# Kernel optimization log

Hardware: AMD Instinct MI355X
Metric: run time of the kernel (lower is better)

## Reference

```python
import jax, jax.numpy as jnp
import numpy as np

MARGIN = 0.2
W_HARD = 1.0
W_SOFT = 0.0
NORMALIZE = True
PD_EPS = 1e-6  # torch F.pairwise_distance eps used inside TripletMarginLoss


def setup_inputs() -> dict:
    key = jax.random.key(0)
    k1, k2, k3 = jax.random.split(key, 3)
    N, D = 8192, 128
    z = jax.random.normal(k1, (N, D), dtype=jnp.float32)
    labels = jax.random.randint(k2, (N,), 0, 16, dtype=jnp.int32)
    subjects = jax.random.randint(k3, (N,), 0, 32, dtype=jnp.int32)
    return {"z": z, "labels": labels, "subjects": subjects}


def _batch_hard(z, pos_mask, neg_mask, margin):
    # pairwise euclidean distances (cdist p=2); mining indices are ints, so
    # stop_gradient keeps vjp clean (matches torch: argmax/argmin detach).
    sq = jnp.sum(z * z, axis=1)
    d2 = sq[:, None] + sq[None, :] - 2.0 * (z @ z.T)
    dist = jax.lax.stop_gradient(jnp.sqrt(jnp.maximum(d2, 0.0)))
    inf = jnp.asarray(jnp.inf, dist.dtype)
    p_idx = jnp.argmax(jnp.where(pos_mask, dist, -inf), axis=1)  # hardest positive
    n_idx = jnp.argmin(jnp.where(neg_mask, dist, inf), axis=1)   # hardest negative
    valid = jnp.any(pos_mask, axis=1) & jnp.any(neg_mask, axis=1)
    a, p, n = z, z[p_idx], z[n_idx]
    d_ap = jnp.sqrt(jnp.sum((a - p + PD_EPS) ** 2, axis=1))
    d_an = jnp.sqrt(jnp.sum((a - n + PD_EPS) ** 2, axis=1))
    per = jnp.maximum(d_ap - d_an + margin, 0.0)
    cnt = jnp.sum(valid)
    loss = jnp.sum(per * valid) / jnp.maximum(cnt, 1).astype(per.dtype)
    return jnp.where(cnt > 0, loss, 0.0)


def reference(z, labels, subjects):
    if NORMALIZE:
        z = z / jnp.maximum(jnp.linalg.norm(z, axis=1, keepdims=True), 1e-12)
    N = z.shape[0]
    same_class = labels[:, None] == labels[None, :]
    same_subj = subjects[:, None] == subjects[None, :]
    not_eye = ~jnp.eye(N, dtype=bool)
    loss = 0.0
    denom = 0.0
    if W_HARD != 0:
        pos_hard = same_class & ~same_subj & not_eye
        neg_hard = ~same_class & same_subj & not_eye
        loss = loss + W_HARD * _batch_hard(z, pos_hard, neg_hard, MARGIN)
        denom += abs(W_HARD)
    if W_SOFT != 0:
        pos_soft = same_class & same_subj & not_eye
        neg_soft = ~same_class & ~same_subj & not_eye
        loss = loss + W_SOFT * _batch_hard(z, pos_soft, neg_soft, MARGIN)
        denom += abs(W_SOFT)
    return loss / max(denom, 1e-12)
```

## Files before the change

kernel.cpp:

```cpp
#include <hip/hip_runtime.h>
#include <math.h>

#define N 8192
#define D 128
#define MARGIN 0.2f
#define PD_EPS 1e-6f
#define CLS_STRIDE 1024
#define SUB_STRIDE 512

typedef __attribute__((ext_vector_type(8))) short bf16x8;
typedef __attribute__((ext_vector_type(4))) float f32x4;

__device__ __forceinline__ unsigned short f2bf(float f) {
    unsigned u = __float_as_uint(f);
    u += 0x7FFFu + ((u >> 16) & 1u);
    return (unsigned short)(u >> 16);
}
__device__ __forceinline__ unsigned umn(unsigned a, unsigned b) { return a < b ? a : b; }
__device__ __forceinline__ unsigned umx(unsigned a, unsigned b) { return a > b ? a : b; }

__global__ __launch_bounds__(256) void k_norm_bucket(const float* __restrict__ z,
                                                     const int* __restrict__ labels,
                                                     const int* __restrict__ subjects,
                                                     unsigned short* __restrict__ znb,
                                                     float* __restrict__ invn,
                                                     int* __restrict__ counters,
                                                     int* __restrict__ clsIdx,
                                                     int* __restrict__ subIdx,
                                                     float* __restrict__ acc) {
    const int b = blockIdx.x;
    const int t = threadIdx.x;
    if (b < 48) {
        const bool isCls = b < 16;
        const int  tgt   = isCls ? b : b - 16;
        const int  wave  = t >> 6, lane = t & 63;
        __shared__ int wbase[4];
        __shared__ int blkbase;
        if (t == 0) blkbase = 0;
        if (b == 0 && t < 3) acc[t] = 0.0f;
        __syncthreads();
        int* dst = isCls ? (clsIdx + tgt * CLS_STRIDE) : (subIdx + tgt * SUB_STRIDE);
        const int stride = isCls ? CLS_STRIDE : SUB_STRIDE;
        for (int base = 0; base < N; base += 256) {
            int row = base + t;
            int lab = labels[row], sub = subjects[row];
            int key   = isCls ? lab : sub;
            int other = isCls ? sub : lab;
            bool pred = (key == tgt);
            unsigned long long mask = __ballot(pred);
            int lrank = __popcll(mask & ((1ull << lane) - 1ull));
            if (lane == 0) wbase[wave] = __popcll(mask);
            __syncthreads();
            int wb = 0;
            #pragma unroll
            for (int w = 0; w < 4; ++w) if (w < wave) wb += wbase[w];
            int chunktot = wbase[0] + wbase[1] + wbase[2] + wbase[3];
            int pos = blkbase + wb + lrank;
            if (pred && pos < stride) dst[pos] = (other << 13) | row;
            __syncthreads();
            if (t == 0) blkbase += chunktot;
        }
        __syncthreads();
        if (t == 0) counters[isCls ? tgt : 16 + tgt] = blkbase;
    } else {
        int row  = (b - 48) * 4 + (t >> 6);
        int lane = t & 63;
        float2 v = ((const float2*)(z + (size_t)row * D))[lane];
        float ss = v.x * v.x + v.y * v.y;
        #pragma unroll
        for (int m = 1; m < 64; m <<= 1) ss += __shfl_xor(ss, m, 64);
        float norm = fmaxf(sqrtf(ss), 1e-12f);
        ushort2 bb; bb.x = f2bf(v.x / norm); bb.y = f2bf(v.y / norm);
        ((ushort2*)(znb + (size_t)row * D))[lane] = bb;
        if (lane == 0) invn[row] = 1.0f / norm;
    }
}

__global__ __launch_bounds__(64, 2) void k_mine(const unsigned short* __restrict__ znb,
                                                const int* __restrict__ counters,
                                                const int* __restrict__ clsIdx,
                                                const int* __restrict__ subIdx,
                                                unsigned* __restrict__ posk,
                                                unsigned* __restrict__ negk) {
    const int b = blockIdx.x;
    const bool isPos = b < 256;
    const int* idx; int cnt, atile;
    if (isPos) {
        int c = b >> 4; atile = b & 15;
        idx = clsIdx + c * CLS_STRIDE;
        cnt = min(counters[c], CLS_STRIDE);
    } else {
        int t = b - 256; int su = t >> 3; atile = t & 7;
        idx = subIdx + su * SUB_STRIDE;
        cnt = min(counters[16 + su], SUB_STRIDE);
    }
    if (atile * 64 >= cnt) return;

    const int lane = threadIdx.x;
    const int m = lane & 15, quad = lane >> 4;

    bf16x8 afrag[4][4];
    #pragma unroll
    for (int u = 0; u < 4; ++u) {
        int sl = min(atile * 64 + u * 16 + m, cnt - 1);
        size_t row = (size_t)(idx[sl] & 8191);
        #pragma unroll
        for (int s = 0; s < 4; ++s)
            afrag[u][s] = *(const bf16x8*)(znb + row * D + s * 32 + quad * 8);
    }
    int cpk[16];
    #pragma unroll
    for (int u = 0; u < 4; ++u)
        #pragma unroll
        for (int r = 0; r < 4; ++r)
            cpk[u * 4 + r] = idx[min(atile * 64 + u * 16 + quad * 4 + r, cnt - 1)];

    unsigned best[16];
    #pragma unroll
    for (int s = 0; s < 16; ++s) best[s] = isPos ? 0xFFFFFFFFu : 0u;

    const int njt = (cnt + 63) >> 6;
    for (int t = 0; t < njt; ++t) {
        int pkB[4];
        #pragma unroll
        for (int v = 0; v < 4; ++v)
            pkB[v] = idx[min(t * 64 + v * 16 + m, cnt - 1)];

        f32x4 acc[4][4];
        #pragma unroll
        for (int u = 0; u < 4; ++u)
            #pragma unroll
            for (int v = 0; v < 4; ++v)
                acc[u][v] = (f32x4){0.f, 0.f, 0.f, 0.f};

        #pragma unroll
        for (int s = 0; s < 4; ++s) {
            bf16x8 bf[4];
            #pragma unroll
            for (int v = 0; v < 4; ++v)
                bf[v] = *(const bf16x8*)(znb + (size_t)(pkB[v] & 8191) * D + s * 32 + quad * 8);
            #pragma unroll
            for (int u = 0; u < 4; ++u)
                #pragma unroll
                for (int v = 0; v < 4; ++v)
                    acc[u][v] = __builtin_amdgcn_mfma_f32_16x16x32_bf16(afrag[u][s], bf[v], acc[u][v], 0, 0, 0);
        }

        #pragma unroll
        for (int v = 0; v < 4; ++v) {
            const unsigned pj = (unsigned)pkB[v];
            #pragma unroll
            for (int u = 0; u < 4; ++u)
                #pragma unroll
                for (int r = 0; r < 4; ++r) {
                    const int s16 = u * 4 + r;
                    unsigned key = (__float_as_uint(acc[u][v][r] + 2.0f) & 0xFFFFE000u) | (pj & 8191u);
                    bool sel = (((unsigned)cpk[s16] ^ pj) & 0xFFFFE000u) != 0u;
                    if (isPos) best[s16] = umn(best[s16], sel ? key : 0xFFFFFFFFu);
                    else       best[s16] = umx(best[s16], sel ? key : 0u);
                }
        }
    }

    #pragma unroll
    for (int mm = 1; mm < 16; mm <<= 1)
        #pragma unroll
        for (int s = 0; s < 16; ++s) {
            unsigned o = (unsigned)__shfl_xor((int)best[s], mm, 64);
            best[s] = isPos ? umn(best[s], o) : umx(best[s], o);
        }
    if (m == 0) {
        unsigned* dst = isPos ? posk : negk;
        #pragma unroll
        for (int s = 0; s < 16; ++s)
            dst[cpk[s] & 8191] = best[s];
    }
}

__global__ __launch_bounds__(256) void k_final(const float* __restrict__ z,
                                               const float* __restrict__ invn,
                                               const unsigned* __restrict__ posk,
                                               const unsigned* __restrict__ negk,
                                               float* __restrict__ acc,
                                               float* __restrict__ out) {
    const int rb = threadIdx.x >> 4;
    const int l  = threadIdx.x & 15;
    const int row = blockIdx.x * 16 + rb;
    unsigned mp = posk[row], mn = negk[row];
    bool valid = (mp != 0xFFFFFFFFu) && (mn != 0u);
    int pi = valid ? (int)(mp & 8191u) : 0;
    int ni = valid ? (int)(mn & 8191u) : 0;
    float ia = invn[row], ip = invn[pi], iq = invn[ni];
    const float4* za = (const float4*)(z + (size_t)row * D);
    const float4* zp = (const float4*)(z + (size_t)pi * D);
    const float4* zq = (const float4*)(z + (size_t)ni * D);
    float sap = 0.f, san = 0.f;
    #pragma unroll
    for (int k = 0; k < 2; ++k) {
        float4 a = za[l * 2 + k], p = zp[l * 2 + k], q = zq[l * 2 + k];
        float d;
        d = a.x * ia - p.x * ip + PD_EPS; sap += d * d;
        d = a.y * ia - p.y * ip + PD_EPS; sap += d * d;
        d = a.z * ia - p.z * ip + PD_EPS; sap += d * d;
        d = a.w * ia - p.w * ip + PD_EPS; sap += d * d;
        d = a.x * ia - q.x * iq + PD_EPS; san += d * d;
        d = a.y * ia - q.y * iq + PD_EPS; san += d * d;
        d = a.z * ia - q.z * iq + PD_EPS; san += d * d;
        d = a.w * ia - q.w * iq + PD_EPS; san += d * d;
    }
    #pragma unroll
    for (int mm = 1; mm < 16; mm <<= 1) {
        sap += __shfl_xor(sap, mm, 64);
        san += __shfl_xor(san, mm, 64);
    }
    __shared__ float ls[16], vs[16];
    if (l == 0) {
        float lo = fmaxf(sqrtf(sap) - sqrtf(san) + MARGIN, 0.0f);
        ls[rb] = valid ? lo : 0.0f;
        vs[rb] = valid ? 1.0f : 0.0f;
    }
    __syncthreads();
    if (threadIdx.x == 0) {
        float s = 0.f, c = 0.f;
        #pragma unroll
        for (int i = 0; i < 16; ++i) { s += ls[i]; c += vs[i]; }
        atomicAdd(&acc[0], s);
        atomicAdd(&acc[1], c);
        __threadfence();
        unsigned old = atomicAdd((unsigned*)&acc[2], 1u);
        if (old == (unsigned)(gridDim.x - 1)) {
            float S = atomicAdd(&acc[0], 0.0f);
            float C = atomicAdd(&acc[1], 0.0f);
            out[0] = (C > 0.f) ? S / fmaxf(C, 1.f) : 0.f;
        }
    }
}

extern "C" void kernel_launch(void* const* d_in, const int* in_sizes, int n_in,
                              void* d_out, int out_size, void* d_ws, size_t ws_size,
                              hipStream_t stream) {
    const float* z        = (const float*)d_in[0];
    const int*   labels   = (const int*)d_in[1];
    const int*   subjects = (const int*)d_in[2];
    float* out = (float*)d_out;

    char* ws = (char*)d_ws;
    unsigned short* znb  = (unsigned short*)(ws);
    float*    invn     = (float*)   (ws + 2097152);
    int*      clsIdx   = (int*)     (ws + 2129920);
    int*      subIdx   = (int*)     (ws + 2195456);
    unsigned* posk     = (unsigned*)(ws + 2260992);
    unsigned* negk     = (unsigned*)(ws + 2293760);
    int*      counters = (int*)     (ws + 2326528);
    float*    acc      = (float*)   (ws + 2326528 + 48 * 4);

    k_norm_bucket<<<dim3(48 + N / 4), dim3(256), 0, stream>>>(z, labels, subjects, znb, invn,
                                                              counters, clsIdx, subIdx, acc);
    k_mine<<<dim3(512), dim3(64), 0, stream>>>(znb, counters, clsIdx, subIdx, posk, negk);
    k_final<<<dim3(N / 16), dim3(256), 0, stream>>>(z, invn, posk, negk, acc, out);
}
```

Measured before the change: 125.2 us.

## Fuse norm, mining and final loss into one cooperative kernel with grid syncs

Merges the three kernels into one cooperative launch of 256 blocks and separates the phases with grid-wide syncs. Work is redistributed per phase: each block normalizes 40 rows, each wave mines one tile, and each block finalizes 32 rows. The bucketing phase also prefetches all labels and subjects into registers up front. This removes two kernel launches and their gaps, but the mining phase now runs as 4 waves per 256-thread block at one block per CU, and grid.sync adds its own overhead.

```diff
diff --git a/kernel.cpp b/kernel.cpp
--- a/kernel.cpp
+++ b/kernel.cpp
@@ -1,5 +1,8 @@
 #include <hip/hip_runtime.h>
+#include <hip/hip_cooperative_groups.h>
 #include <math.h>
+
+namespace cg = cooperative_groups;
 
 #define N 8192
 #define D 128
@@ -19,219 +22,236 @@
 __device__ __forceinline__ unsigned umn(unsigned a, unsigned b) { return a < b ? a : b; }
 __device__ __forceinline__ unsigned umx(unsigned a, unsigned b) { return a > b ? a : b; }
 
-__global__ __launch_bounds__(256) void k_norm_bucket(const float* __restrict__ z,
-                                                     const int* __restrict__ labels,
-                                                     const int* __restrict__ subjects,
-                                                     unsigned short* __restrict__ znb,
-                                                     float* __restrict__ invn,
-                                                     int* __restrict__ counters,
-                                                     int* __restrict__ clsIdx,
-                                                     int* __restrict__ subIdx,
-                                                     float* __restrict__ acc) {
+__global__ __launch_bounds__(256, 1) void k_fused(const float* __restrict__ z,
+                                                  const int* __restrict__ labels,
+                                                  const int* __restrict__ subjects,
+                                                  unsigned short* __restrict__ znb,
+                                                  float* __restrict__ invn,
+                                                  int* __restrict__ counters,
+                                                  int* __restrict__ clsIdx,
+                                                  int* __restrict__ subIdx,
+                                                  unsigned* __restrict__ posk,
+                                                  unsigned* __restrict__ negk,
+                                                  float* __restrict__ acc,
+                                                  float* __restrict__ out) {
+    cg::grid_group grid = cg::this_grid();
     const int b = blockIdx.x;
     const int t = threadIdx.x;
+    const int wave = t >> 6, lane = t & 63;
+
+    __shared__ int wcnt[4];
+    __shared__ int blkbase;
+    __shared__ float ls[16], vs[16];
+
     if (b < 48) {
         const bool isCls = b < 16;
         const int  tgt   = isCls ? b : b - 16;
-        const int  wave  = t >> 6, lane = t & 63;
-        __shared__ int wbase[4];
-        __shared__ int blkbase;
+        int keyv[32], otherv[32];
+        #pragma unroll
+        for (int r = 0; r < 32; ++r) {
+            int row = r * 256 + t;
+            int lab = labels[row], sub = subjects[row];
+            keyv[r]   = isCls ? lab : sub;
+            otherv[r] = isCls ? sub : lab;
+        }
+        if (b == 0 && t < 3) acc[t] = 0.0f;
         if (t == 0) blkbase = 0;
-        if (b == 0 && t < 3) acc[t] = 0.0f;
         __syncthreads();
         int* dst = isCls ? (clsIdx + tgt * CLS_STRIDE) : (subIdx + tgt * SUB_STRIDE);
         const int stride = isCls ? CLS_STRIDE : SUB_STRIDE;
-        for (int base = 0; base < N; base += 256) {
-            int row = base + t;
-            int lab = labels[row], sub = subjects[row];
-            int key   = isCls ? lab : sub;
-            int other = isCls ? sub : lab;
-            bool pred = (key == tgt);
+        #pragma unroll
+        for (int r = 0; r < 32; ++r) {
+            bool pred = (keyv[r] == tgt);
             unsigned long long mask = __ballot(pred);
             int lrank = __popcll(mask & ((1ull << lane) - 1ull));
-            if (lane == 0) wbase[wave] = __popcll(mask);
+            if (lane == 0) wcnt[wave] = __popcll(mask);
             __syncthreads();
             int wb = 0;
             #pragma unroll
-            for (int w = 0; w < 4; ++w) if (w < wave) wb += wbase[w];
-            int chunktot = wbase[0] + wbase[1] + wbase[2] + wbase[3];
+            for (int w = 0; w < 4; ++w) if (w < wave) wb += wcnt[w];
+            int tot = wcnt[0] + wcnt[1] + wcnt[2] + wcnt[3];
             int pos = blkbase + wb + lrank;
-            if (pred && pos < stride) dst[pos] = (other << 13) | row;
+            if (pred && pos < stride) dst[pos] = (otherv[r] << 13) | (r * 256 + t);
             __syncthreads();
-            if (t == 0) blkbase += chunktot;
+            if (t == 0) blkbase += tot;
         }
         __syncthreads();
         if (t == 0) counters[isCls ? tgt : 16 + tgt] = blkbase;
     } else {
-        int row  = (b - 48) * 4 + (t >> 6);
-        int lane = t & 63;
-        float2 v = ((const float2*)(z + (size_t)row * D))[lane];
-        float ss = v.x * v.x + v.y * v.y;
+        for (int p = 0; p < 10; ++p) {
+            int row = (b - 48) * 40 + p * 4 + wave;
+            if (row < N) {
+                float2 v = ((const float2*)(z + (size_t)row * D))[lane];
+                float ss = v.x * v.x + v.y * v.y;
+                #pragma unroll
+                for (int m = 1; m < 64; m <<= 1) ss += __shfl_xor(ss, m, 64);
+                float norm = fmaxf(sqrtf(ss), 1e-12f);
+                ushort2 bb; bb.x = f2bf(v.x / norm); bb.y = f2bf(v.y / norm);
+                ((ushort2*)(znb + (size_t)row * D))[lane] = bb;
+                if (lane == 0) invn[row] = 1.0f / norm;
+            }
+        }
+    }
+
+    grid.sync();
+
+    {
+        const int gw = b * 4 + wave;
+        bool active = gw < 512;
+        const int* idx = nullptr; int cnt = 0, atile = 0; bool isPos = false;
+        if (active) {
+            isPos = gw < 256;
+            if (isPos) {
+                int c = gw >> 4; atile = gw & 15;
+                idx = clsIdx + c * CLS_STRIDE;
+                cnt = min(counters[c], CLS_STRIDE);
+            } else {
+                int tt = gw - 256; int su = tt >> 3; atile = tt & 7;
+                idx = subIdx + su * SUB_STRIDE;
+                cnt = min(counters[16 + su], SUB_STRIDE);
+            }
+            if (atile * 64 >= cnt) active = false;
+        }
+        if (active) {
+            const int m = lane & 15, quad = lane >> 4;
+
+            bf16x8 afrag[4][4];
+            #pragma unroll
+            for (int u = 0; u < 4; ++u) {
+                int sl = min(atile * 64 + u * 16 + m, cnt - 1);
+                size_t row = (size_t)(idx[sl] & 8191);
+                #pragma unroll
+                for (int s = 0; s < 4; ++s)
+                    afrag[u][s] = *(const bf16x8*)(znb + row * D + s * 32 + quad * 8);
+            }
+            int cpk[16];
+            #pragma unroll
+            for (int u = 0; u < 4; ++u)
+                #pragma unroll
+                for (int r = 0; r < 4; ++r)
+                    cpk[u * 4 + r] = idx[min(atile * 64 + u * 16 + quad * 4 + r, cnt - 1)];
+
+            unsigned best[16];
+            #pragma unroll
+            for (int s = 0; s < 16; ++s) best[s] = isPos ? 0xFFFFFFFFu : 0u;
+
+            const int njt = (cnt + 63) >> 6;
+            for (int tt = 0; tt < njt; ++tt) {
+                int pkB[4];
+                #pragma unroll
+                for (int v = 0; v < 4; ++v)
+                    pkB[v] = idx[min(tt * 64 + v * 16 + m, cnt - 1)];
+
+                f32x4 ac[4][4];
+                #pragma unroll
+                for (int u = 0; u < 4; ++u)
+                    #pragma unroll
+                    for (int v = 0; v < 4; ++v)
+                        ac[u][v] = (f32x4){0.f, 0.f, 0.f, 0.f};
+
+                #pragma unroll
+                for (int s = 0; s < 4; ++s) {
+                    bf16x8 bf[4];
+                    #pragma unroll
+                    for (int v = 0; v < 4; ++v)
+                        bf[v] = *(const bf16x8*)(znb + (size_t)(pkB[v] & 8191) * D + s * 32 + quad * 8);
+                    #pragma unroll
+                    for (int u = 0; u < 4; ++u)
+                        #pragma unroll
+                        for (int v = 0; v < 4; ++v)
+                            ac[u][v] = __builtin_amdgcn_mfma_f32_16x16x32_bf16(afrag[u][s], bf[v], ac[u][v], 0, 0, 0);
+                }
+
+                #pragma unroll
+                for (int v = 0; v < 4; ++v) {
+                    const unsigned pj = (unsigned)pkB[v];
+                    #pragma unroll
+                    for (int u = 0; u < 4; ++u)
+                        #pragma unroll
+                        for (int r = 0; r < 4; ++r) {
+                            const int s16 = u * 4 + r;
+                            unsigned key = (__float_as_uint(ac[u][v][r] + 2.0f) & 0xFFFFE000u) | (pj & 8191u);
+                            bool sel = (((unsigned)cpk[s16] ^ pj) & 0xFFFFE000u) != 0u;
+                            if (isPos) best[s16] = umn(best[s16], sel ? key : 0xFFFFFFFFu);
+                            else       best[s16] = umx(best[s16], sel ? key : 0u);
+                        }
+                }
+            }
+
+            #pragma unroll
+            for (int mm = 1; mm < 16; mm <<= 1)
+                #pragma unroll
+                for (int s = 0; s < 16; ++s) {
+                    unsigned o = (unsigned)__shfl_xor((int)best[s], mm, 64);
+                    best[s] = isPos ? umn(best[s], o) : umx(best[s], o);
+                }
+            if (m == 0) {
+                unsigned* dstk = isPos ? posk : negk;
+                #pragma unroll
+                for (int s = 0; s < 16; ++s)
+                    dstk[cpk[s] & 8191] = best[s];
+            }
+        }
+    }
+
+    grid.sync();
+
+    {
+        const int rb = t >> 4;
+        const int l  = t & 15;
+        float lsum = 0.f, vsum = 0.f;
         #pragma unroll
-        for (int m = 1; m < 64; m <<= 1) ss += __shfl_xor(ss, m, 64);
-        float norm = fmaxf(sqrtf(ss), 1e-12f);
-        ushort2 bb; bb.x = f2bf(v.x / norm); bb.y = f2bf(v.y / norm);
-        ((ushort2*)(znb + (size_t)row * D))[lane] = bb;
-        if (lane == 0) invn[row] = 1.0f / norm;
-    }
-}
-
-__global__ __launch_bounds__(64, 2) void k_mine(const unsigned short* __restrict__ znb,
-                                                const int* __restrict__ counters,
-                                                const int* __restrict__ clsIdx,
-                                                const int* __restrict__ subIdx,
-                                                unsigned* __restrict__ posk,
-                                                unsigned* __restrict__ negk) {
-    const int b = blockIdx.x;
-    const bool isPos = b < 256;
-    const int* idx; int cnt, atile;
-    if (isPos) {
-        int c = b >> 4; atile = b & 15;
-        idx = clsIdx + c * CLS_STRIDE;
-        cnt = min(counters[c], CLS_STRIDE);
-    } else {
-        int t = b - 256; int su = t >> 3; atile = t & 7;
-        idx = subIdx + su * SUB_STRIDE;
-        cnt = min(counters[16 + su], SUB_STRIDE);
-    }
-    if (atile * 64 >= cnt) return;
-
-    const int lane = threadIdx.x;
-    const int m = lane & 15, quad = lane >> 4;
-
-    bf16x8 afrag[4][4];
-    #pragma unroll
-    for (int u = 0; u < 4; ++u) {
-        int sl = min(atile * 64 + u * 16 + m, cnt - 1);
-        size_t row = (size_t)(idx[sl] & 8191);
-        #pragma unroll
-        for (int s = 0; s < 4; ++s)
-            afrag[u][s] = *(const bf16x8*)(znb + row * D + s * 32 + quad * 8);
-    }
-    int cpk[16];
-    #pragma unroll
-    for (int u = 0; u < 4; ++u)
-        #pragma unroll
-        for (int r = 0; r < 4; ++r)
-            cpk[u * 4 + r] = idx[min(atile * 64 + u * 16 + quad * 4 + r, cnt - 1)];
-
-    unsigned best[16];
-    #pragma unroll
-    for (int s = 0; s < 16; ++s) best[s] = isPos ? 0xFFFFFFFFu : 0u;
-
-    const int njt = (cnt + 63) >> 6;
-    for (int t = 0; t < njt; ++t) {
-        int pkB[4];
-        #pragma unroll
-        for (int v = 0; v < 4; ++v)
-            pkB[v] = idx[min(t * 64 + v * 16 + m, cnt - 1)];
-
-        f32x4 acc[4][4];
-        #pragma unroll
-        for (int u = 0; u < 4; ++u)
-            #pragma unroll
-            for (int v = 0; v < 4; ++v)
-                acc[u][v] = (f32x4){0.f, 0.f, 0.f, 0.f};
-
-        #pragma unroll
-        for (int s = 0; s < 4; ++s) {
-            bf16x8 bf[4];
-            #pragma unroll
-            for (int v = 0; v < 4; ++v)
-                bf[v] = *(const bf16x8*)(znb + (size_t)(pkB[v] & 8191) * D + s * 32 + quad * 8);
-            #pragma unroll
-            for (int u = 0; u < 4; ++u)
-                #pragma unroll
-                for (int v = 0; v < 4; ++v)
-                    acc[u][v] = __builtin_amdgcn_mfma_f32_16x16x32_bf16(afrag[u][s], bf[v], acc[u][v], 0, 0, 0);
-        }
-
-        #pragma unroll
-        for (int v = 0; v < 4; ++v) {
-            const unsigned pj = (unsigned)pkB[v];
-            #pragma unroll
-            for (int u = 0; u < 4; ++u)
-                #pragma unroll
-                for (int r = 0; r < 4; ++r) {
-                    const int s16 = u * 4 + r;
-                    unsigned key = (__float_as_uint(acc[u][v][r] + 2.0f) & 0xFFFFE000u) | (pj & 8191u);
-                    bool sel = (((unsigned)cpk[s16] ^ pj) & 0xFFFFE000u) != 0u;
-                    if (isPos) best[s16] = umn(best[s16], sel ? key : 0xFFFFFFFFu);
-                    else       best[s16] = umx(best[s16], sel ? key : 0u);
-                }
-        }
-    }
-
-    #pragma unroll
-    for (int mm = 1; mm < 16; mm <<= 1)
-        #pragma unroll
-        for (int s = 0; s < 16; ++s) {
-            unsigned o = (unsigned)__shfl_xor((int)best[s], mm, 64);
-            best[s] = isPos ? umn(best[s], o) : umx(best[s], o);
-        }
-    if (m == 0) {
-        unsigned* dst = isPos ? posk : negk;
-        #pragma unroll
-        for (int s = 0; s < 16; ++s)
-            dst[cpk[s] & 8191] = best[s];
-    }
-}
-
-__global__ __launch_bounds__(256) void k_final(const float* __restrict__ z,
-                                               const float* __restrict__ invn,
-                                               const unsigned* __restrict__ posk,
-                                               const unsigned* __restrict__ negk,
-                                               float* __restrict__ acc,
-                                               float* __restrict__ out) {
-    const int rb = threadIdx.x >> 4;
-    const int l  = threadIdx.x & 15;
-    const int row = blockIdx.x * 16 + rb;
-    unsigned mp = posk[row], mn = negk[row];
-    bool valid = (mp != 0xFFFFFFFFu) && (mn != 0u);
-    int pi = valid ? (int)(mp & 8191u) : 0;
-    int ni = valid ? (int)(mn & 8191u) : 0;
-    float ia = invn[row], ip = invn[pi], iq = invn[ni];
-    const float4* za = (const float4*)(z + (size_t)row * D);
-    const float4* zp = (const float4*)(z + (size_t)pi * D);
-    const float4* zq = (const float4*)(z + (size_t)ni * D);
-    float sap = 0.f, san = 0.f;
-    #pragma unroll
-    for (int k = 0; k < 2; ++k) {
-        float4 a = za[l * 2 + k], p = zp[l * 2 + k], q = zq[l * 2 + k];
-        float d;
-        d = a.x * ia - p.x * ip + PD_EPS; sap += d * d;
-        d = a.y * ia - p.y * ip + PD_EPS; sap += d * d;
-        d = a.z * ia - p.z * ip + PD_EPS; sap += d * d;
-        d = a.w * ia - p.w * ip + PD_EPS; sap += d * d;
-        d = a.x * ia - q.x * iq + PD_EPS; san += d * d;
-        d = a.y * ia - q.y * iq + PD_EPS; san += d * d;
-        d = a.z * ia - q.z * iq + PD_EPS; san += d * d;
-        d = a.w * ia - q.w * iq + PD_EPS; san += d * d;
-    }
-    #pragma unroll
-    for (int mm = 1; mm < 16; mm <<= 1) {
-        sap += __shfl_xor(sap, mm, 64);
-        san += __shfl_xor(san, mm, 64);
-    }
-    __shared__ float ls[16], vs[16];
-    if (l == 0) {
-        float lo = fmaxf(sqrtf(sap) - sqrtf(san) + MARGIN, 0.0f);
-        ls[rb] = valid ? lo : 0.0f;
-        vs[rb] = valid ? 1.0f : 0.0f;
-    }
-    __syncthreads();
-    if (threadIdx.x == 0) {
-        float s = 0.f, c = 0.f;
-        #pragma unroll
-        for (int i = 0; i < 16; ++i) { s += ls[i]; c += vs[i]; }
-        atomicAdd(&acc[0], s);
-        atomicAdd(&acc[1], c);
-        __threadfence();
-        unsigned old = atomicAdd((unsigned*)&acc[2], 1u);
-        if (old == (unsigned)(gridDim.x - 1)) {
-            float S = atomicAdd(&acc[0], 0.0f);
-            float C = atomicAdd(&acc[1], 0.0f);
-            out[0] = (C > 0.f) ? S / fmaxf(C, 1.f) : 0.f;
+        for (int p = 0; p < 2; ++p) {
+            const int row = b * 32 + p * 16 + rb;
+            unsigned mp = posk[row], mn = negk[row];
+            bool valid = (mp != 0xFFFFFFFFu) && (mn != 0u);
+            int pi = valid ? (int)(mp & 8191u) : 0;
+            int ni = valid ? (int)(mn & 8191u) : 0;
+            float ia = invn[row], ip = invn[pi], iq = invn[ni];
+            const float4* za = (const float4*)(z + (size_t)row * D);
+            const float4* zp = (const float4*)(z + (size_t)pi * D);
+            const float4* zq = (const float4*)(z + (size_t)ni * D);
+            float sap = 0.f, san = 0.f;
+            #pragma unroll
+            for (int k = 0; k < 2; ++k) {
+                float4 a = za[l * 2 + k], pp = zp[l * 2 + k], qq = zq[l * 2 + k];
+                float d;
+                d = a.x * ia - pp.x * ip + PD_EPS; sap += d * d;
+                d = a.y * ia - pp.y * ip + PD_EPS; sap += d * d;
+                d = a.z * ia - pp.z * ip + PD_EPS; sap += d * d;
+                d = a.w * ia - pp.w * ip + PD_EPS; sap += d * d;
+                d = a.x * ia - qq.x * iq + PD_EPS; san += d * d;
+                d = a.y * ia - qq.y * iq + PD_EPS; san += d * d;
+                d = a.z * ia - qq.z * iq + PD_EPS; san += d * d;
+                d = a.w * ia - qq.w * iq + PD_EPS; san += d * d;
+            }
+            #pragma unroll
+            for (int mm = 1; mm < 16; mm <<= 1) {
+                sap += __shfl_xor(sap, mm, 64);
+                san += __shfl_xor(san, mm, 64);
+            }
+            if (l == 0) {
+                float lo = fmaxf(sqrtf(sap) - sqrtf(san) + MARGIN, 0.0f);
+                lsum += valid ? lo : 0.0f;
+                vsum += valid ? 1.0f : 0.0f;
+            }
+        }
+        __syncthreads();
+        if (l == 0) { ls[rb] = lsum; vs[rb] = vsum; }
+        __syncthreads();
+        if (t == 0) {
+            float s = 0.f, c = 0.f;
+            #pragma unroll
+            for (int i = 0; i < 16; ++i) { s += ls[i]; c += vs[i]; }
+            atomicAdd(&acc[0], s);
+            atomicAdd(&acc[1], c);
+            __threadfence();
+            unsigned old = atomicAdd((unsigned*)&acc[2], 1u);
+            if (old == (unsigned)(gridDim.x - 1)) {
+                float S = atomicAdd(&acc[0], 0.0f);
+                float C = atomicAdd(&acc[1], 0.0f);
+                out[0] = (C > 0.f) ? S / fmaxf(C, 1.f) : 0.f;
+            }
         }
     }
 }
@@ -254,8 +274,8 @@
     int*      counters = (int*)     (ws + 2326528);
     float*    acc      = (float*)   (ws + 2326528 + 48 * 4);
 
-    k_norm_bucket<<<dim3(48 + N / 4), dim3(256), 0, stream>>>(z, labels, subjects, znb, invn,
-                                                              counters, clsIdx, subIdx, acc);
-    k_mine<<<dim3(512), dim3(64), 0, stream>>>(znb, counters, clsIdx, subIdx, posk, negk);
-    k_final<<<dim3(N / 16), dim3(256), 0, stream>>>(z, invn, posk, negk, acc, out);
+    void* args[] = {(void*)&z, (void*)&labels, (void*)&subjects, (void*)&znb,
+                    (void*)&invn, (void*)&counters, (void*)&clsIdx, (void*)&subIdx,
+                    (void*)&posk, (void*)&negk, (void*)&acc, (void*)&out};
+    hipLaunchCooperativeKernel((const void*)k_fused, dim3(256), dim3(256), args, 0, stream);
 }
```

After: 177.9 us. 1.42x slower.
